# Kernel tuning notes

Hardware: AMD Instinct MI355X
Metric: run time of the kernel (lower is better)

The kernel has to match this reference:

```python
import jax, jax.numpy as jnp
import numpy as np

K = 6
STRIDE = 2

def _conv1d(x, w, b):
    # x: [B,1,L], w: [1,1,K] (OIW), b: [1]
    y = jax.lax.conv_general_dilated(
        x, w, window_strides=(STRIDE,), padding='VALID',
        dimension_numbers=('NCW', 'OIW', 'NCW'))
    return y + b[None, :, None]

def setup_inputs() -> dict:
    key = jax.random.key(0)
    kx, k1, k2, k3, kb1, kb2, kb3 = jax.random.split(key, 7)
    bound = 1.0 / np.sqrt(1 * K)  # torch Conv1d default init bound
    x = jax.random.normal(kx, (4096, 1, 16384), dtype=jnp.float32)
    w1 = jax.random.uniform(k1, (1, 1, K), jnp.float32, -bound, bound)
    w2 = jax.random.uniform(k2, (1, 1, K), jnp.float32, -bound, bound)
    w3 = jax.random.uniform(k3, (1, 1, K), jnp.float32, -bound, bound)
    b1 = jax.random.uniform(kb1, (1,), jnp.float32, -bound, bound)
    b2 = jax.random.uniform(kb2, (1,), jnp.float32, -bound, bound)
    b3 = jax.random.uniform(kb3, (1,), jnp.float32, -bound, bound)
    return {"x": x, "w1": w1, "b1": b1, "w2": w2, "b2": b2, "w3": w3, "b3": b3}

def reference(x, w1, b1, w2, b2, w3, b3):
    # three stacked strided valid convs, matching torch Encoder.forward
    x = _conv1d(x, w1, b1)  # [B,1,8190]
    x = _conv1d(x, w2, b2)  # [B,1,4093]
    x = _conv1d(x, w3, b3)  # [B,1,2044]
    return x
```

## Files before the change

kernel.cpp:

```cpp
#include <hip/hip_runtime.h>
#include <hip/hip_bf16.h>


#define L_IN  16384
#define L1    8190
#define L2    4093
#define L3    2044
#define KW    6

__global__ __launch_bounds__(256) void encoder_fused_kernel(
    const float* __restrict__ x,
    const float* __restrict__ w1, const float* __restrict__ b1,
    const float* __restrict__ w2, const float* __restrict__ b2,
    const float* __restrict__ w3, const float* __restrict__ b3,
    float* __restrict__ out)
{
    const int j3 = blockIdx.x * blockDim.x + threadIdx.x;
    const int row = blockIdx.y;
    if (j3 >= L3) return;

    float W1[KW], W2[KW], W3[KW];
#pragma unroll
    for (int t = 0; t < KW; ++t) { W1[t] = w1[t]; W2[t] = w2[t]; W3[t] = w3[t]; }
    const float B1 = b1[0], B2 = b2[0], B3 = b3[0];

    const float* xr = x + (size_t)row * L_IN + 8 * (size_t)j3;
    float v[36];
    const float4* xv = reinterpret_cast<const float4*>(xr);
#pragma unroll
    for (int i = 0; i < 9; ++i) {
        float4 t = xv[i];
        v[4 * i + 0] = t.x;
        v[4 * i + 1] = t.y;
        v[4 * i + 2] = t.z;
        v[4 * i + 3] = t.w;
    }

    float c1[16];
#pragma unroll
    for (int i = 0; i < 16; ++i) {
        float s = B1;
#pragma unroll
        for (int t = 0; t < KW; ++t) s = fmaf(W1[t], v[2 * i + t], s);
        c1[i] = s;
    }

    float c2[KW];
#pragma unroll
    for (int i = 0; i < KW; ++i) {
        float s = B2;
#pragma unroll
        for (int t = 0; t < KW; ++t) s = fmaf(W2[t], c1[2 * i + t], s);
        c2[i] = s;
    }

    float o = B3;
#pragma unroll
    for (int t = 0; t < KW; ++t) o = fmaf(W3[t], c2[t], o);

    out[(size_t)row * L3 + j3] = o;
}

extern "C" void kernel_launch(void* const* d_in, const int* in_sizes, int n_in,
                              void* d_out, int out_size, void* d_ws, size_t ws_size,
                              hipStream_t stream) {
    const float* x  = (const float*)d_in[0];
    const float* w1 = (const float*)d_in[1];
    const float* b1 = (const float*)d_in[2];
    const float* w2 = (const float*)d_in[3];
    const float* b2 = (const float*)d_in[4];
    const float* w3 = (const float*)d_in[5];
    const float* b3 = (const float*)d_in[6];
    float* out = (float*)d_out;

    const int B = in_sizes[0] / L_IN;

    dim3 block(256);
    dim3 grid((L3 + 255) / 256, B);
    encoder_fused_kernel<<<grid, block, 0, stream>>>(x, w1, b1, w2, b2, w3, b3, out);
}
```

Measured before the change: 368.5 us.

## Collapse three stacked convolutions into one 36-tap strided filter, four outputs per thread

Composes the three linear stride-2 convolutions into a single 36-tap stride-8 filter with a combined bias, computed per block in shared memory. Each thread now produces four consecutive outputs from 60 loaded inputs and writes them as one float4, replacing the per-output recomputation of the layer-1 and layer-2 intermediates. This reduces redundant input loads and FMAs, since the before version read 36 inputs per single output. Each block adds a small prologue and a barrier, and the summation order changes, which can alter floating-point rounding slightly.

```diff
diff --git a/kernel.cpp b/kernel.cpp
--- a/kernel.cpp
+++ b/kernel.cpp
@@ -3,10 +3,9 @@
 
 
 #define L_IN  16384
-#define L1    8190
-#define L2    4093
 #define L3    2044
 #define KW    6
+#define GROUPS (L3 / 4)
 
 __global__ __launch_bounds__(256) void encoder_fused_kernel(
     const float* __restrict__ x,
@@ -15,50 +14,60 @@
     const float* __restrict__ w3, const float* __restrict__ b3,
     float* __restrict__ out)
 {
-    const int j3 = blockIdx.x * blockDim.x + threadIdx.x;
+    __shared__ float sW[37];
+
+    const int tx = threadIdx.x;
+    if (tx < 36) {
+        float s = 0.f;
+        for (int a = 0; a < KW; ++a) {
+            const int rem = tx - 4 * a;
+            for (int b = 0; b < KW; ++b) {
+                const int c = rem - 2 * b;
+                if (c >= 0 && c < KW) s += w3[a] * w2[b] * w1[c];
+            }
+        }
+        sW[tx] = s;
+    } else if (tx == 36) {
+        float s3 = 0.f, s2 = 0.f;
+        for (int i = 0; i < KW; ++i) { s3 += w3[i]; s2 += w2[i]; }
+        sW[36] = b3[0] + b2[0] * s3 + b1[0] * s2 * s3;
+    }
+    __syncthreads();
+
+    const int t = blockIdx.x * blockDim.x + tx;
     const int row = blockIdx.y;
-    if (j3 >= L3) return;
+    if (t >= GROUPS) return;
+    const int j3 = 4 * t;
 
-    float W1[KW], W2[KW], W3[KW];
+    float W[36];
 #pragma unroll
-    for (int t = 0; t < KW; ++t) { W1[t] = w1[t]; W2[t] = w2[t]; W3[t] = w3[t]; }
-    const float B1 = b1[0], B2 = b2[0], B3 = b3[0];
+    for (int k = 0; k < 36; ++k) W[k] = sW[k];
+    const float Beff = sW[36];
 
     const float* xr = x + (size_t)row * L_IN + 8 * (size_t)j3;
-    float v[36];
     const float4* xv = reinterpret_cast<const float4*>(xr);
+    float v[60];
 #pragma unroll
-    for (int i = 0; i < 9; ++i) {
-        float4 t = xv[i];
-        v[4 * i + 0] = t.x;
-        v[4 * i + 1] = t.y;
-        v[4 * i + 2] = t.z;
-        v[4 * i + 3] = t.w;
+    for (int i = 0; i < 15; ++i) {
+        float4 q = xv[i];
+        v[4 * i + 0] = q.x;
+        v[4 * i + 1] = q.y;
+        v[4 * i + 2] = q.z;
+        v[4 * i + 3] = q.w;
     }
 
-    float c1[16];
+    float acc[4];
 #pragma unroll
-    for (int i = 0; i < 16; ++i) {
-        float s = B1;
+    for (int i = 0; i < 4; ++i) {
+        float s = Beff;
 #pragma unroll
-        for (int t = 0; t < KW; ++t) s = fmaf(W1[t], v[2 * i + t], s);
-        c1[i] = s;
+        for (int k = 0; k < 36; ++k) s = fmaf(W[k], v[8 * i + k], s);
+        acc[i] = s;
     }
 
-    float c2[KW];
-#pragma unroll
-    for (int i = 0; i < KW; ++i) {
-        float s = B2;
-#pragma unroll
-        for (int t = 0; t < KW; ++t) s = fmaf(W2[t], c1[2 * i + t], s);
-        c2[i] = s;
-    }
-
-    float o = B3;
-#pragma unroll
-    for (int t = 0; t < KW; ++t) o = fmaf(W3[t], c2[t], o);
-
-    out[(size_t)row * L3 + j3] = o;
+    float4 o;
+    o.x = acc[0]; o.y = acc[1]; o.z = acc[2]; o.w = acc[3];
+    *reinterpret_cast<float4*>(out + (size_t)row * L3 + j3) = o;
 }
 
 extern "C" void kernel_launch(void* const* d_in, const int* in_sizes, int n_in,
@@ -76,6 +85,6 @@
     const int B = in_sizes[0] / L_IN;
 
     dim3 block(256);
-    dim3 grid((L3 + 255) / 256, B);
+    dim3 grid((GROUPS + 255) / 256, B);
     encoder_fused_kernel<<<grid, block, 0, stream>>>(x, w1, b1, w2, b2, w3, b3, out);
 }
```

After: 399.5 us. +8.4%, slower.
